# Optimization experiments

Measured on AMD Instinct MI355X. Metric: run time of the kernel, lower is better.

Reference implementation:

```python
import jax, jax.numpy as jnp
import numpy as np

VOCAB, EMB, HID = 10000, 512, 512
B, T = 32, 256


def _lstm_layer(x, W, U, b):
    # x: [B, T, D_in]; W: [D_in, 4H]; U: [H, 4H]; b: [4H]
    Bsz = x.shape[0]
    H = U.shape[0]
    xs = jnp.swapaxes(x, 0, 1)  # [T, B, D_in]

    def step(carry, xt):
        h, c = carry
        z = xt @ W + h @ U + b  # fused gate GEMM, [B, 4H]
        i, f, g, o = jnp.split(z, 4, axis=-1)
        i = jax.nn.sigmoid(i)
        f = jax.nn.sigmoid(f)
        g = jnp.tanh(g)
        o = jax.nn.sigmoid(o)
        c = f * c + i * g
        h = o * jnp.tanh(c)
        return (h, c), h

    init = (jnp.zeros((Bsz, H), x.dtype), jnp.zeros((Bsz, H), x.dtype))
    _, hs = jax.lax.scan(step, init, xs)  # hs: [T, B, H]
    return jnp.swapaxes(hs, 0, 1)  # [B, T, H]


def setup_inputs() -> dict:
    key = jax.random.key(0)
    ks = jax.random.split(key, 10)
    s = 1.0 / np.sqrt(HID)
    inp = {
        "tokens": jax.random.randint(ks[0], (B, T), 0, VOCAB, dtype=jnp.int32),
        "embedding": jax.random.normal(ks[1], (VOCAB, EMB), jnp.float32) * 0.02,
        "W0": jax.random.uniform(ks[2], (EMB, 4 * HID), jnp.float32, -s, s),
        "U0": jax.random.uniform(ks[3], (HID, 4 * HID), jnp.float32, -s, s),
        "b0": jnp.zeros((4 * HID,), jnp.float32),
        "W1": jax.random.uniform(ks[4], (HID, 4 * HID), jnp.float32, -s, s),
        "U1": jax.random.uniform(ks[5], (HID, 4 * HID), jnp.float32, -s, s),
        "b1": jnp.zeros((4 * HID,), jnp.float32),
        "W_out": jax.random.normal(ks[6], (HID, VOCAB), jnp.float32) * 0.02,
        "b_out": jnp.zeros((VOCAB,), jnp.float32),
    }
    return inp


def reference(tokens, embedding, W0, U0, b0, W1, U1, b1, W_out, b_out):
    x = embedding[tokens]            # [B, T, EMB]
    x = _lstm_layer(x, W0, U0, b0)   # [B, T, H]
    x = _lstm_layer(x, W1, U1, b1)   # [B, T, H]
    y = x.reshape(-1, HID) @ W_out + b_out  # [B*T, VOCAB]
    return y
```

## Files before the change

### kernel.cpp

```cpp
#include <hip/hip_runtime.h>
#include <math.h>

#define B_    32
#define T_    256
#define HID_  512
#define G4_   2048
#define VOC_  10000
#define NPAD_ 10112

typedef float f32x4 __attribute__((ext_vector_type(4)));
typedef short bf16x8 __attribute__((ext_vector_type(8)));
typedef unsigned short u16;
typedef u16 u16x8 __attribute__((ext_vector_type(8)));

#define AADD(p)  __hip_atomic_fetch_add((p), 1u, __ATOMIC_RELAXED, __HIP_MEMORY_SCOPE_AGENT)
#define ALOAD(p) __hip_atomic_load((p), __ATOMIC_RELAXED, __HIP_MEMORY_SCOPE_AGENT)

__device__ __forceinline__ void load4_coherent(const float* p0, const float* p1,
                                               const float* p2, const float* p3,
                                               f32x4& a, f32x4& b, f32x4& c, f32x4& d)
{
    asm volatile(
        "global_load_dwordx4 %0, %4, off sc0 sc1\n\t"
        "global_load_dwordx4 %1, %5, off sc0 sc1\n\t"
        "global_load_dwordx4 %2, %6, off sc0 sc1\n\t"
        "global_load_dwordx4 %3, %7, off sc0 sc1\n\t"
        "s_waitcnt vmcnt(0)"
        : "=&v"(a), "=&v"(b), "=&v"(c), "=&v"(d)
        : "v"(p0), "v"(p1), "v"(p2), "v"(p3)
        : "memory");
}
__device__ __forceinline__ void store_coherent(float* p, float x)
{
    asm volatile("global_store_dword %0, %1, off sc0 sc1" :: "v"(p), "v"(x) : "memory");
}

__device__ __forceinline__ float fsigm(float x)
{
    float e = exp2f(x * -1.4426950408889634f);
    return __builtin_amdgcn_rcpf(1.f + e);
}
__device__ __forceinline__ float ftanh(float x)
{
    float e = exp2f(x * 2.8853900817779268f);
    return 1.f - 2.f * __builtin_amdgcn_rcpf(e + 1.f);
}

__device__ __forceinline__ void bsplit(float x, u16& hi, u16& lo)
{
    union { float f; unsigned u; } a; a.f = x;
    unsigned r = a.u + 0x7FFFu + ((a.u >> 16) & 1u);
    hi = (u16)(r >> 16);
    union { unsigned u; float f; } hf; hf.u = ((unsigned)hi) << 16;
    union { float f; unsigned u; } b; b.f = x - hf.f;
    unsigned r2 = b.u + 0x7FFFu + ((b.u >> 16) & 1u);
    lo = (u16)(r2 >> 16);
}

__device__ __forceinline__ void wait_ge(unsigned* p, unsigned tgt)
{
    unsigned g = 0;
    while (ALOAD(p) < tgt) {
        __builtin_amdgcn_s_sleep(2);
        if (++g > 100000000u) break;
    }
}

__global__ __launch_bounds__(256)
void wsplit_k(const float* __restrict__ W, u16* __restrict__ Thi,
              u16* __restrict__ Tlo, int N)
{
    __shared__ float tile[64][68];
    const int tid = threadIdx.x;
    const int n0 = blockIdx.x * 64;
    const int k0 = blockIdx.y * 64;

    #pragma unroll
    for (int it = 0; it < 4; ++it) {
        int idx = it * 256 + tid;
        int kr = idx >> 4;
        int nc = (idx & 15) * 4;
        int n  = n0 + nc;
        float4 v = {0.f, 0.f, 0.f, 0.f};
        const float* wp = W + (size_t)(k0 + kr) * N + n;
        if (n + 3 < N) v = *(const float4*)wp;
        else {
            if (n + 0 < N) v.x = wp[0];
            if (n + 1 < N) v.y = wp[1];
            if (n + 2 < N) v.z = wp[2];
            if (n + 3 < N) v.w = wp[3];
        }
        tile[kr][nc + 0] = v.x; tile[kr][nc + 1] = v.y;
        tile[kr][nc + 2] = v.z; tile[kr][nc + 3] = v.w;
    }
    __syncthreads();

    #pragma unroll
    for (int it = 0; it < 2; ++it) {
        int idx = it * 256 + tid;
        int nr = idx >> 3;
        int kb = (idx & 7) * 8;
        u16x8 hv, lv;
        #pragma unroll
        for (int e = 0; e < 8; ++e) {
            u16 h, l;
            bsplit(tile[kb + e][nr], h, l);
            hv[e] = h; lv[e] = l;
        }
        size_t o = (size_t)(n0 + nr) * 512 + k0 + kb;
        *(u16x8*)(Thi + o) = hv;
        *(u16x8*)(Tlo + o) = lv;
    }
}

__global__ __launch_bounds__(256)
void gather_split_k(const int* __restrict__ tokens, const float* __restrict__ emb,
                    u16* __restrict__ Ahi, u16* __restrict__ Alo)
{
    const int r    = blockIdx.x * 4 + (threadIdx.x >> 6);
    const int lane = threadIdx.x & 63;
    const int tok  = tokens[(r & 31) * T_ + (r >> 5)];
    const float* src = emb + (size_t)tok * 512 + lane * 8;
    float4 v0 = *(const float4*)(src);
    float4 v1 = *(const float4*)(src + 4);
    const float vv[8] = {v0.x, v0.y, v0.z, v0.w, v1.x, v1.y, v1.z, v1.w};
    u16x8 hv, lv;
    #pragma unroll
    for (int e = 0; e < 8; ++e) { u16 h, l; bsplit(vv[e], h, l); hv[e] = h; lv[e] = l; }
    size_t o = (size_t)r * 512 + lane * 8;
    *(u16x8*)(Ahi + o) = hv;
    *(u16x8*)(Alo + o) = lv;
}

template<int MODE>
__global__ __launch_bounds__(256)
void gemm_bf16_k(const u16* __restrict__ Ahi, const u16* __restrict__ Alo,
                 const u16* __restrict__ Bhi, const u16* __restrict__ Blo,
                 const float* __restrict__ bias, float* __restrict__ C, int N)
{
    __shared__ u16 As[2][128 * 64];
    __shared__ u16 Bs[2][128 * 64];

    const int tid  = threadIdx.x;
    const int lane = tid & 63;
    const int wid  = tid >> 6;
    const int wm   = wid >> 1;
    const int wn   = wid & 1;
    const int m0   = blockIdx.y * 128;
    const int n0   = blockIdx.x * 128;

    f32x4 acc[4][4];
    #pragma unroll
    for (int i = 0; i < 4; ++i)
        #pragma unroll
        for (int j = 0; j < 4; ++j) acc[i][j] = (f32x4){0.f, 0.f, 0.f, 0.f};

    auto stage = [&](int s, int buf) {
        const int ksel = s >> 3;
        const int koff = (s & 7) * 64;
        const u16* Asrc = (ksel == 2) ? Alo : Ahi;
        const u16* Bsrc = (ksel == 1) ? Blo : Bhi;
        #pragma unroll
        for (int q = 0; q < 4; ++q) {
            const int u   = q * 256 + tid;
            const int row = u >> 3;
            const int kch = (u & 7) ^ (row & 7);
            const u16* ga = Asrc + (size_t)(m0 + row) * 512 + koff + kch * 8;
            const u16* gb = Bsrc + (size_t)(n0 + row) * 512 + koff + kch * 8;
            u16* la = &As[buf][(q * 256 + wid * 64) * 8];
            u16* lb = &Bs[buf][(q * 256 + wid * 64) * 8];
            __builtin_amdgcn_global_load_lds(
                (const __attribute__((address_space(1))) void*)ga,
                (__attribute__((address_space(3))) void*)la, 16, 0, 0);
            __builtin_amdgcn_global_load_lds(
                (const __attribute__((address_space(1))) void*)gb,
                (__attribute__((address_space(3))) void*)lb, 16, 0, 0);
        }
    };

    stage(0, 0);
    for (int s = 0; s < 24; ++s) {
        const int buf = s & 1;
        __syncthreads();
        if (s + 1 < 24) stage(s + 1, buf ^ 1);

        #pragma unroll
        for (int q = 0; q < 2; ++q) {
            bf16x8 af[4], bfr[4];
            #pragma unroll
            for (int mt = 0; mt < 4; ++mt) {
                const int r    = wm * 64 + mt * 16 + (lane & 15);
                const int slot = (q * 4 + (lane >> 4)) ^ (r & 7);
                af[mt] = *(const bf16x8*)&As[buf][r * 64 + slot * 8];
            }
            #pragma unroll
            for (int nt = 0; nt < 4; ++nt) {
                const int rn   = wn * 64 + nt * 16 + (lane & 15);
                const int slot = (q * 4 + (lane >> 4)) ^ (rn & 7);
                bfr[nt] = *(const bf16x8*)&Bs[buf][rn * 64 + slot * 8];
            }
            #pragma unroll
            for (int mt = 0; mt < 4; ++mt)
                #pragma unroll
                for (int nt = 0; nt < 4; ++nt)
                    acc[mt][nt] = __builtin_amdgcn_mfma_f32_16x16x32_bf16(
                        af[mt], bfr[nt], acc[mt][nt], 0, 0, 0);
        }
    }

    #pragma unroll
    for (int mt = 0; mt < 4; ++mt) {
        #pragma unroll
        for (int nt = 0; nt < 4; ++nt) {
            const int c = n0 + wn * 64 + nt * 16 + (lane & 15);
            #pragma unroll
            for (int j = 0; j < 4; ++j) {
                const int r = m0 + wm * 64 + mt * 16 + (lane >> 4) * 4 + j;
                float val = acc[mt][nt][j];
                if constexpr (MODE == 0) {
                    val += bias[c];
                    const int t = r >> 5, bgrp = (r >> 3) & 3, bb = r & 7;
                    const int g = c >> 9, jblk = (c & 511) >> 3, jjs = c & 7;
                    C[(((size_t)t * 4 + bgrp) * 64 + jblk) * 256 + bb * 32 + g * 8 + jjs] = val;
                } else {
                    if (c < VOC_) {
                        val += bias[c];
                        const size_t orow = (size_t)(r & 31) * T_ + (r >> 5);
                        C[orow * VOC_ + c] = val;
                    }
                }
            }
        }
    }
}

__global__ __launch_bounds__(256, 2)
void fused_rec_k(const float* __restrict__ G, const float* __restrict__ U0,
                 const float* __restrict__ W1, const float* __restrict__ U1,
                 const float* __restrict__ b1,
                 float* __restrict__ H0x,
                 u16* __restrict__ Ahi, u16* __restrict__ Alo,
                 float* __restrict__ h1buf,
                 unsigned* __restrict__ bar)
{
    __shared__ float lds[8 * 1152];

    const int tid  = threadIdx.x;
    const int role = blockIdx.x >> 8;
    const int blk  = blockIdx.x & 255;
    const int bg   = blk >> 6;
    const int cgr  = blk & 63;
    const int j0   = cgr * 8;
    const int b0   = bg * 8;

    const int jj  = tid >> 5;
    const int kc  = tid & 31;
    const int g_  = kc >> 3;
    const int bb_ = kc & 7;
    const int shard = cgr & 3;

    unsigned* shard0 = bar + (bg * 4 + shard) * 16;
    unsigned* root0  = bar + 256 + bg * 16;
    unsigned* shard1 = bar + 512 + (bg * 4 + shard) * 16;
    unsigned* root1  = bar + 768 + bg * 16;

    if (role == 0) {
        float u[4][16];
        #pragma unroll
        for (int g = 0; g < 4; ++g)
            #pragma unroll
            for (int kk = 0; kk < 16; ++kk)
                u[g][kk] = U0[(size_t)(kc * 16 + kk) * G4_ + (g << 9) + j0 + jj];

        const int gofs = bb_ * 32 + g_ * 8 + jj;
        float zpre = G[((size_t)bg * 64 + cgr) * 256 + gofs];
        float c_reg = 0.f;

        for (int t = 0; t < T_; ++t) {
            if (tid == 0 && t > 0) wait_ge(root0, 4u * (unsigned)t);
            __syncthreads();

            {
                const float* p[4]; float* dst[4];
                const float* hcur = H0x + (size_t)t * (B_ * HID_);
                #pragma unroll
                for (int q = 0; q < 4; ++q) {
                    int idx = q * 256 + tid;
                    int bL  = idx >> 7;
                    int k4  = idx & 127;
                    p[q]   = hcur + (b0 + bL) * HID_ + k4 * 4;
                    dst[q] = &lds[bL * 640 + (k4 >> 2) * 20 + (k4 & 3) * 4];
                }
                f32x4 v0, v1, v2, v3;
                load4_coherent(p[0], p[1], p[2], p[3], v0, v1, v2, v3);
                *(f32x4*)dst[0] = v0; *(f32x4*)dst[1] = v1;
                *(f32x4*)dst[2] = v2; *(f32x4*)dst[3] = v3;
            }
            __syncthreads();

            float zpre_next = 0.f;
            if (t + 1 < T_)
                zpre_next = G[((size_t)((t + 1) * 4 + bg) * 64 + cgr) * 256 + gofs];

            float v[32];
            #pragma unroll
            for (int s = 0; s < 32; ++s) v[s] = 0.f;
            #pragma unroll
            for (int bb = 0; bb < 8; ++bb) {
                const float* hp = &lds[bb * 640 + kc * 20];
                f32x4 h0v = *(const f32x4*)(hp + 0);
                f32x4 h1v = *(const f32x4*)(hp + 4);
                f32x4 h2v = *(const f32x4*)(hp + 8);
                f32x4 h3v = *(const f32x4*)(hp + 12);
                const float hh[16] = {h0v.x, h0v.y, h0v.z, h0v.w, h1v.x, h1v.y, h1v.z, h1v.w,
                                      h2v.x, h2v.y, h2v.z, h2v.w, h3v.x, h3v.y, h3v.z, h3v.w};
                #pragma unroll
                for (int g = 0; g < 4; ++g)
                    #pragma unroll
                    for (int kk = 0; kk < 16; ++kk)
                        v[g * 8 + bb] += u[g][kk] * hh[kk];
            }

            float a16[16];
            #pragma unroll
            for (int i = 0; i < 16; ++i) {
                float keep = (kc & 16) ? v[i + 16] : v[i];
                float give = (kc & 16) ? v[i]      : v[i + 16];
                a16[i] = keep + __shfl_xor(give, 16, 32);
            }
            float a8[8];
            #pragma unroll
            for (int i = 0; i < 8; ++i) {
                float keep = (kc & 8) ? a16[i + 8] : a16[i];
                float give = (kc & 8) ? a16[i]     : a16[i + 8];
                a8[i] = keep + __shfl_xor(give, 8, 32);
            }
            float a4[4];
            #pragma unroll
            for (int i = 0; i < 4; ++i) {
                float keep = (kc & 4) ? a8[i + 4] : a8[i];
                float give = (kc & 4) ? a8[i]     : a8[i + 4];
                a4[i] = keep + __shfl_xor(give, 4, 32);
            }
            float a2[2];
            #pragma unroll
            for (int i = 0; i < 2; ++i) {
                float keep = (kc & 2) ? a4[i + 2] : a4[i];
                float give = (kc & 2) ? a4[i]     : a4[i + 2];
                a2[i] = keep + __shfl_xor(give, 2, 32);
            }
            float keep1 = (kc & 1) ? a2[1] : a2[0];
            float give1 = (kc & 1) ? a2[0] : a2[1];
            float z = keep1 + __shfl_xor(give1, 1, 32) + zpre;
            zpre = zpre_next;

            float z8  = __shfl_xor(z, 8, 32);
            float z16 = __shfl_xor(z, 16, 32);
            float z24 = __shfl_xor(z, 24, 32);
            float i_ = fsigm(z);
            float f_ = fsigm(z8);
            float gg = ftanh(z16);
            float o_ = fsigm(z24);
            c_reg = f_ * c_reg + i_ * gg;
            float h_ = o_ * ftanh(c_reg);

            if (g_ == 0)
                store_coherent(&H0x[(size_t)(t + 1) * (B_ * HID_)
                                    + (b0 + bb_) * HID_ + j0 + jj], h_);

            __syncthreads();
            if (tid == 0) {
                unsigned old = AADD(shard0);
                if (old + 1u == 16u * (unsigned)(t + 1)) AADD(root0);
            }
        }
    } else {
        float u[4][32];
        #pragma unroll
        for (int g = 0; g < 4; ++g)
            #pragma unroll
            for (int kk = 0; kk < 32; ++kk) {
                const int K = kc * 32 + kk;
                u[g][kk] = (K < 512)
                    ? W1[(size_t)K * G4_ + (g << 9) + j0 + jj]
                    : U1[(size_t)(K - 512) * G4_ + (g << 9) + j0 + jj];
            }
        const float zb = b1[(g_ << 9) + j0 + jj];
        float c_reg = 0.f;

        for (int t = 0; t < T_; ++t) {
            if (tid == 0) {
                wait_ge(root0, 4u * (unsigned)(t + 1));
                if (t > 0) wait_ge(root1, 4u * (unsigned)t);
            }
            __syncthreads();

            {
                const float* xbase = H0x  + (size_t)(t + 1) * (B_ * HID_);
                const float* hbase = h1buf + (size_t)(t & 1) * (B_ * HID_);
                const float* p[8]; float* dst[8];
                const int k = tid * 4;
                #pragma unroll
                for (int q = 0; q < 8; ++q) {
                    p[q] = (k < 512) ? (xbase + (b0 + q) * HID_ + k)
                                     : (hbase + (b0 + q) * HID_ + (k - 512));
                    dst[q] = &lds[q * 1152 + (tid >> 3) * 36 + (tid & 7) * 4];
                }
                f32x4 v0, v1, v2, v3, v4, v5, v6, v7;
                load4_coherent(p[0], p[1], p[2], p[3], v0, v1, v2, v3);
                load4_coherent(p[4], p[5], p[6], p[7], v4, v5, v6, v7);
                *(f32x4*)dst[0] = v0; *(f32x4*)dst[1] = v1;
                *(f32x4*)dst[2] = v2; *(f32x4*)dst[3] = v3;
                *(f32x4*)dst[4] = v4; *(f32x4*)dst[5] = v5;
                *(f32x4*)dst[6] = v6; *(f32x4*)dst[7] = v7;
            }
            __syncthreads();

            float v[32];
            #pragma unroll
            for (int s = 0; s < 32; ++s) v[s] = 0.f;
            #pragma unroll
            for (int bb = 0; bb < 8; ++bb) {
                const float* hp = &lds[bb * 1152 + kc * 36];
                #pragma unroll
                for (int half = 0; half < 2; ++half) {
                    f32x4 h0v = *(const f32x4*)(hp + half * 16 + 0);
                    f32x4 h1v = *(const f32x4*)(hp + half * 16 + 4);
                    f32x4 h2v = *(const f32x4*)(hp + half * 16 + 8);
                    f32x4 h3v = *(const f32x4*)(hp + half * 16 + 12);
                    const float hh[16] = {h0v.x, h0v.y, h0v.z, h0v.w, h1v.x, h1v.y, h1v.z, h1v.w,
                                          h2v.x, h2v.y, h2v.z, h2v.w, h3v.x, h3v.y, h3v.z, h3v.w};
                    #pragma unroll
                    for (int g = 0; g < 4; ++g)
                        #pragma unroll
                        for (int kk = 0; kk < 16; ++kk)
                            v[g * 8 + bb] += u[g][half * 16 + kk] * hh[kk];
                }
            }

            float a16[16];
            #pragma unroll
            for (int i = 0; i < 16; ++i) {
                float keep = (kc & 16) ? v[i + 16] : v[i];
                float give = (kc & 16) ? v[i]      : v[i + 16];
                a16[i] = keep + __shfl_xor(give, 16, 32);
            }
            float a8[8];
            #pragma unroll
            for (int i = 0; i < 8; ++i) {
                float keep = (kc & 8) ? a16[i + 8] : a16[i];
                float give = (kc & 8) ? a16[i]     : a16[i + 8];
                a8[i] = keep + __shfl_xor(give, 8, 32);
            }
            float a4[4];
            #pragma unroll
            for (int i = 0; i < 4; ++i) {
                float keep = (kc & 4) ? a8[i + 4] : a8[i];
                float give = (kc & 4) ? a8[i]     : a8[i + 4];
                a4[i] = keep + __shfl_xor(give, 4, 32);
            }
            float a2[2];
            #pragma unroll
            for (int i = 0; i < 2; ++i) {
                float keep = (kc & 2) ? a4[i + 2] : a4[i];
                float give = (kc & 2) ? a4[i]     : a4[i + 2];
                a2[i] = keep + __shfl_xor(give, 2, 32);
            }
            float keep1 = (kc & 1) ? a2[1] : a2[0];
            float give1 = (kc & 1) ? a2[0] : a2[1];
            float z = keep1 + __shfl_xor(give1, 1, 32) + zb;

            float z8  = __shfl_xor(z, 8, 32);
            float z16 = __shfl_xor(z, 16, 32);
            float z24 = __shfl_xor(z, 24, 32);
            float i_ = fsigm(z);
            float f_ = fsigm(z8);
            float gg = ftanh(z16);
            float o_ = fsigm(z24);
            c_reg = f_ * c_reg + i_ * gg;
            float h_ = o_ * ftanh(c_reg);

            if (g_ == 0) {
                const int brow = b0 + bb_;
                store_coherent(&h1buf[(size_t)((t + 1) & 1) * (B_ * HID_)
                                      + brow * HID_ + j0 + jj], h_);
                u16 hi, lo; bsplit(h_, hi, lo);
                const size_t o = ((size_t)t * B_ + brow) * HID_ + j0 + jj;
                Ahi[o] = hi;
                Alo[o] = lo;
            }

            __syncthreads();
            if (tid == 0) {
                unsigned old = AADD(shard1);
                if (old + 1u == 16u * (unsigned)(t + 1)) AADD(root1);
            }
        }
    }
}

extern "C" void kernel_launch(void* const* d_in, const int* in_sizes, int n_in,
                              void* d_out, int out_size, void* d_ws, size_t ws_size,
                              hipStream_t stream)
{
    const int*   tokens = (const int*)  d_in[0];
    const float* emb    = (const float*)d_in[1];
    const float* W0     = (const float*)d_in[2];
    const float* U0     = (const float*)d_in[3];
    const float* b0     = (const float*)d_in[4];
    const float* W1     = (const float*)d_in[5];
    const float* U1     = (const float*)d_in[6];
    const float* b1     = (const float*)d_in[7];
    const float* Wout   = (const float*)d_in[8];
    const float* bout   = (const float*)d_in[9];
    float* out = (float*)d_out;

    float* G   = out;
    float* H0x = out + (size_t)8192 * 2048;

    u16* ws16 = (u16*)d_ws;
    size_t o = 0;
    u16* Ahi   = ws16 + o; o += (size_t)8192 * 512;
    u16* Alo   = ws16 + o; o += (size_t)8192 * 512;
    u16* W0Thi = ws16 + o; o += (size_t)G4_ * 512;
    u16* W0Tlo = ws16 + o; o += (size_t)G4_ * 512;
    u16* WoThi = ws16 + o; o += (size_t)NPAD_ * 512;
    u16* WoTlo = ws16 + o; o += (size_t)NPAD_ * 512;
    float*    h1buf = (float*)(ws16 + o);
    unsigned* bar   = (unsigned*)(h1buf + 2 * B_ * HID_);

    dim3 blk(256);

    wsplit_k<<<dim3(G4_ / 64, 8), blk, 0, stream>>>(W0, W0Thi, W0Tlo, G4_);
    wsplit_k<<<dim3(NPAD_ / 64, 8), blk, 0, stream>>>(Wout, WoThi, WoTlo, VOC_);
    gather_split_k<<<dim3(2048), blk, 0, stream>>>(tokens, emb, Ahi, Alo);

    gemm_bf16_k<0><<<dim3(G4_ / 128, 64), blk, 0, stream>>>(
        Ahi, Alo, W0Thi, W0Tlo, b0, G, G4_);

    hipMemsetAsync(H0x, 0, B_ * HID_ * sizeof(float), stream);
    hipMemsetAsync(h1buf, 0, B_ * HID_ * sizeof(float), stream);
    hipMemsetAsync(bar, 0, 1024 * sizeof(unsigned), stream);
    fused_rec_k<<<dim3(512), blk, 0, stream>>>(
        G, U0, W1, U1, b1, H0x, Ahi, Alo, h1buf, bar);

    gemm_bf16_k<1><<<dim3(NPAD_ / 128, 64), blk, 0, stream>>>(
        Ahi, Alo, WoThi, WoTlo, bout, out, NPAD_);
}
```

Before: 2.215 ms.

## Split layer-1 recurrence into separate input-projection and recurrent roles

The persistent recurrent kernel gains a third role. New blocks compute the layer-1 input projection x_t@W1+b1 into a G1 buffer, pipelined behind layer 0, so the layer-1 recurrent blocks only do h@U1 with half the K dimension. This shortens the critical path of the serial layer-1 recurrence. In exchange it launches 768 blocks at 3 per CU, which needs all of them co-resident for the spin barriers, and it adds extra global traffic and synchronization through G1.

```diff
diff --git a/kernel.cpp b/kernel.cpp
--- a/kernel.cpp
+++ b/kernel.cpp
@@ -7,6 +7,7 @@
 #define G4_   2048
 #define VOC_  10000
 #define NPAD_ 10112
+#define BH_   (B_ * HID_)
 
 typedef float f32x4 __attribute__((ext_vector_type(4)));
 typedef short bf16x8 __attribute__((ext_vector_type(8)));
@@ -29,6 +30,13 @@
         : "=&v"(a), "=&v"(b), "=&v"(c), "=&v"(d)
         : "v"(p0), "v"(p1), "v"(p2), "v"(p3)
         : "memory");
+}
+__device__ __forceinline__ float load_coherent_f32(const float* p)
+{
+    float v;
+    asm volatile("global_load_dword %0, %1, off sc0 sc1\n\ts_waitcnt vmcnt(0)"
+                 : "=v"(v) : "v"(p) : "memory");
+    return v;
 }
 __device__ __forceinline__ void store_coherent(float* p, float x)
 {
@@ -234,16 +242,17 @@
     }
 }
 
-__global__ __launch_bounds__(256, 2)
-void fused_rec_k(const float* __restrict__ G, const float* __restrict__ U0,
-                 const float* __restrict__ W1, const float* __restrict__ U1,
-                 const float* __restrict__ b1,
-                 float* __restrict__ H0x,
-                 u16* __restrict__ Ahi, u16* __restrict__ Alo,
-                 float* __restrict__ h1buf,
-                 unsigned* __restrict__ bar)
-{
-    __shared__ float lds[8 * 1152];
+__global__ __launch_bounds__(256, 3)
+void rec3_k(const float* __restrict__ G, const float* __restrict__ U0,
+            const float* __restrict__ W1, const float* __restrict__ U1,
+            const float* __restrict__ b1,
+            float* __restrict__ H0x,
+            float* __restrict__ G1,
+            u16* __restrict__ Ahi, u16* __restrict__ Alo,
+            float* __restrict__ h1buf,
+            unsigned* __restrict__ bar)
+{
+    __shared__ float lds[8 * 640];
 
     const int tid  = threadIdx.x;
     const int role = blockIdx.x >> 8;
@@ -257,102 +266,116 @@
     const int kc  = tid & 31;
     const int g_  = kc >> 3;
     const int bb_ = kc & 7;
-    const int shard = cgr & 3;
-
-    unsigned* shard0 = bar + (bg * 4 + shard) * 16;
-    unsigned* root0  = bar + 256 + bg * 16;
-    unsigned* shard1 = bar + 512 + (bg * 4 + shard) * 16;
-    unsigned* root1  = bar + 768 + bg * 16;
+    const int gofs = bb_ * 32 + g_ * 8 + jj;
+
+    unsigned* baseA = bar + (0 * 4 + bg) * 80;
+    unsigned* baseB = bar + (1 * 4 + bg) * 80;
+    unsigned* baseC = bar + (2 * 4 + bg) * 80;
+    unsigned* mybase  = (role == 0) ? baseA : (role == 1) ? baseB : baseC;
+    unsigned* myshard = mybase + (cgr & 3) * 16;
+    unsigned* myroot  = mybase + 64;
+    unsigned* rootA = baseA + 64;
+    unsigned* rootB = baseB + 64;
+    unsigned* rootC = baseC + 64;
+
+    const float* Usrc = (role == 0) ? U0 : (role == 1) ? W1 : U1;
+    float u[4][16];
+    #pragma unroll
+    for (int g = 0; g < 4; ++g)
+        #pragma unroll
+        for (int kk = 0; kk < 16; ++kk)
+            u[g][kk] = Usrc[(size_t)(kc * 16 + kk) * G4_ + (g << 9) + j0 + jj];
+
+    auto stage_tile = [&](const float* src) {
+        const float* p[4]; float* dst[4];
+        #pragma unroll
+        for (int q = 0; q < 4; ++q) {
+            int idx = q * 256 + tid;
+            int bL  = idx >> 7;
+            int k4  = idx & 127;
+            p[q]   = src + (b0 + bL) * HID_ + k4 * 4;
+            dst[q] = &lds[bL * 640 + (k4 >> 2) * 20 + (k4 & 3) * 4];
+        }
+        f32x4 v0, v1, v2, v3;
+        load4_coherent(p[0], p[1], p[2], p[3], v0, v1, v2, v3);
+        *(f32x4*)dst[0] = v0; *(f32x4*)dst[1] = v1;
+        *(f32x4*)dst[2] = v2; *(f32x4*)dst[3] = v3;
+    };
+
+    auto dot_reduce = [&]() -> float {
+        float v[32];
+        #pragma unroll
+        for (int s = 0; s < 32; ++s) v[s] = 0.f;
+        #pragma unroll
+        for (int bb = 0; bb < 8; ++bb) {
+            const float* hp = &lds[bb * 640 + kc * 20];
+            f32x4 h0v = *(const f32x4*)(hp + 0);
+            f32x4 h1v = *(const f32x4*)(hp + 4);
+            f32x4 h2v = *(const f32x4*)(hp + 8);
+            f32x4 h3v = *(const f32x4*)(hp + 12);
+            const float hh[16] = {h0v.x, h0v.y, h0v.z, h0v.w, h1v.x, h1v.y, h1v.z, h1v.w,
+                                  h2v.x, h2v.y, h2v.z, h2v.w, h3v.x, h3v.y, h3v.z, h3v.w};
+            #pragma unroll
+            for (int g = 0; g < 4; ++g)
+                #pragma unroll
+                for (int kk = 0; kk < 16; ++kk)
+                    v[g * 8 + bb] += u[g][kk] * hh[kk];
+        }
+        float a16[16];
+        #pragma unroll
+        for (int i = 0; i < 16; ++i) {
+            float keep = (kc & 16) ? v[i + 16] : v[i];
+            float give = (kc & 16) ? v[i]      : v[i + 16];
+            a16[i] = keep + __shfl_xor(give, 16, 32);
+        }
+        float a8[8];
+        #pragma unroll
+        for (int i = 0; i < 8; ++i) {
+            float keep = (kc & 8) ? a16[i + 8] : a16[i];
+            float give = (kc & 8) ? a16[i]     : a16[i + 8];
+            a8[i] = keep + __shfl_xor(give, 8, 32);
+        }
+        float a4[4];
+        #pragma unroll
+        for (int i = 0; i < 4; ++i) {
+            float keep = (kc & 4) ? a8[i + 4] : a8[i];
+            float give = (kc & 4) ? a8[i]     : a8[i + 4];
+            a4[i] = keep + __shfl_xor(give, 4, 32);
+        }
+        float a2[2];
+        #pragma unroll
+        for (int i = 0; i < 2; ++i) {
+            float keep = (kc & 2) ? a4[i + 2] : a4[i];
+            float give = (kc & 2) ? a4[i]     : a4[i + 2];
+            a2[i] = keep + __shfl_xor(give, 2, 32);
+        }
+        float keep1 = (kc & 1) ? a2[1] : a2[0];
+        float give1 = (kc & 1) ? a2[0] : a2[1];
+        return keep1 + __shfl_xor(give1, 1, 32);
+    };
+
+    auto arrive = [&](int t) {
+        if (tid == 0) {
+            unsigned old = AADD(myshard);
+            if (old + 1u == 16u * (unsigned)(t + 1)) AADD(myroot);
+        }
+    };
 
     if (role == 0) {
-        float u[4][16];
-        #pragma unroll
-        for (int g = 0; g < 4; ++g)
-            #pragma unroll
-            for (int kk = 0; kk < 16; ++kk)
-                u[g][kk] = U0[(size_t)(kc * 16 + kk) * G4_ + (g << 9) + j0 + jj];
-
-        const int gofs = bb_ * 32 + g_ * 8 + jj;
         float zpre = G[((size_t)bg * 64 + cgr) * 256 + gofs];
         float c_reg = 0.f;
-
         for (int t = 0; t < T_; ++t) {
-            if (tid == 0 && t > 0) wait_ge(root0, 4u * (unsigned)t);
-            __syncthreads();
-
-            {
-                const float* p[4]; float* dst[4];
-                const float* hcur = H0x + (size_t)t * (B_ * HID_);
-                #pragma unroll
-                for (int q = 0; q < 4; ++q) {
-                    int idx = q * 256 + tid;
-                    int bL  = idx >> 7;
-                    int k4  = idx & 127;
-                    p[q]   = hcur + (b0 + bL) * HID_ + k4 * 4;
-                    dst[q] = &lds[bL * 640 + (k4 >> 2) * 20 + (k4 & 3) * 4];
-                }
-                f32x4 v0, v1, v2, v3;
-                load4_coherent(p[0], p[1], p[2], p[3], v0, v1, v2, v3);
-                *(f32x4*)dst[0] = v0; *(f32x4*)dst[1] = v1;
-                *(f32x4*)dst[2] = v2; *(f32x4*)dst[3] = v3;
-            }
-            __syncthreads();
-
-            float zpre_next = 0.f;
+            if (tid == 0 && t > 0) wait_ge(rootA, 4u * (unsigned)t);
+            __syncthreads();
+            stage_tile(H0x + (size_t)t * BH_);
+            __syncthreads();
+
+            float zpn = 0.f;
             if (t + 1 < T_)
-                zpre_next = G[((size_t)((t + 1) * 4 + bg) * 64 + cgr) * 256 + gofs];
-
-            float v[32];
-            #pragma unroll
-            for (int s = 0; s < 32; ++s) v[s] = 0.f;
-            #pragma unroll
-            for (int bb = 0; bb < 8; ++bb) {
-                const float* hp = &lds[bb * 640 + kc * 20];
-                f32x4 h0v = *(const f32x4*)(hp + 0);
-                f32x4 h1v = *(const f32x4*)(hp + 4);
-                f32x4 h2v = *(const f32x4*)(hp + 8);
-                f32x4 h3v = *(const f32x4*)(hp + 12);
-                const float hh[16] = {h0v.x, h0v.y, h0v.z, h0v.w, h1v.x, h1v.y, h1v.z, h1v.w,
-                                      h2v.x, h2v.y, h2v.z, h2v.w, h3v.x, h3v.y, h3v.z, h3v.w};
-                #pragma unroll
-                for (int g = 0; g < 4; ++g)
-                    #pragma unroll
-                    for (int kk = 0; kk < 16; ++kk)
-                        v[g * 8 + bb] += u[g][kk] * hh[kk];
-            }
-
-            float a16[16];
-            #pragma unroll
-            for (int i = 0; i < 16; ++i) {
-                float keep = (kc & 16) ? v[i + 16] : v[i];
-                float give = (kc & 16) ? v[i]      : v[i + 16];
-                a16[i] = keep + __shfl_xor(give, 16, 32);
-            }
-            float a8[8];
-            #pragma unroll
-            for (int i = 0; i < 8; ++i) {
-                float keep = (kc & 8) ? a16[i + 8] : a16[i];
-                float give = (kc & 8) ? a16[i]     : a16[i + 8];
-                a8[i] = keep + __shfl_xor(give, 8, 32);
-            }
-            float a4[4];
-            #pragma unroll
-            for (int i = 0; i < 4; ++i) {
-                float keep = (kc & 4) ? a8[i + 4] : a8[i];
-                float give = (kc & 4) ? a8[i]     : a8[i + 4];
-                a4[i] = keep + __shfl_xor(give, 4, 32);
-            }
-            float a2[2];
-            #pragma unroll
-            for (int i = 0; i < 2; ++i) {
-                float keep = (kc & 2) ? a4[i + 2] : a4[i];
-                float give = (kc & 2) ? a4[i]     : a4[i + 2];
-                a2[i] = keep + __shfl_xor(give, 2, 32);
-            }
-            float keep1 = (kc & 1) ? a2[1] : a2[0];
-            float give1 = (kc & 1) ? a2[0] : a2[1];
-            float z = keep1 + __shfl_xor(give1, 1, 32) + zpre;
-            zpre = zpre_next;
+                zpn = G[(((size_t)(t + 1) * 4 + bg) * 64 + cgr) * 256 + gofs];
+
+            float z = dot_reduce() + zpre;
+            zpre = zpn;
 
             float z8  = __shfl_xor(z, 8, 32);
             float z16 = __shfl_xor(z, 16, 32);
@@ -365,110 +388,39 @@
             float h_ = o_ * ftanh(c_reg);
 
             if (g_ == 0)
-                store_coherent(&H0x[(size_t)(t + 1) * (B_ * HID_)
-                                    + (b0 + bb_) * HID_ + j0 + jj], h_);
-
-            __syncthreads();
-            if (tid == 0) {
-                unsigned old = AADD(shard0);
-                if (old + 1u == 16u * (unsigned)(t + 1)) AADD(root0);
-            }
+                store_coherent(&H0x[(size_t)(t + 1) * BH_ + (b0 + bb_) * HID_ + j0 + jj], h_);
+
+            __syncthreads();
+            arrive(t);
+        }
+    } else if (role == 1) {
+        const float zb = b1[(g_ << 9) + j0 + jj];
+        for (int t = 0; t < T_; ++t) {
+            if (tid == 0) wait_ge(rootA, 4u * (unsigned)(t + 1));
+            __syncthreads();
+            stage_tile(H0x + (size_t)(t + 1) * BH_);
+            __syncthreads();
+
+            float z = dot_reduce() + zb;
+            store_coherent(&G1[(((size_t)t * 4 + bg) * 64 + cgr) * 256 + gofs], z);
+
+            __syncthreads();
+            arrive(t);
         }
     } else {
-        float u[4][32];
-        #pragma unroll
-        for (int g = 0; g < 4; ++g)
-            #pragma unroll
-            for (int kk = 0; kk < 32; ++kk) {
-                const int K = kc * 32 + kk;
-                u[g][kk] = (K < 512)
-                    ? W1[(size_t)K * G4_ + (g << 9) + j0 + jj]
-                    : U1[(size_t)(K - 512) * G4_ + (g << 9) + j0 + jj];
-            }
-        const float zb = b1[(g_ << 9) + j0 + jj];
         float c_reg = 0.f;
-
         for (int t = 0; t < T_; ++t) {
             if (tid == 0) {
-                wait_ge(root0, 4u * (unsigned)(t + 1));
-                if (t > 0) wait_ge(root1, 4u * (unsigned)t);
+                wait_ge(rootB, 4u * (unsigned)(t + 1));
+                if (t > 0) wait_ge(rootC, 4u * (unsigned)t);
             }
             __syncthreads();
-
-            {
-                const float* xbase = H0x  + (size_t)(t + 1) * (B_ * HID_);
-                const float* hbase = h1buf + (size_t)(t & 1) * (B_ * HID_);
-                const float* p[8]; float* dst[8];
-                const int k = tid * 4;
-                #pragma unroll
-                for (int q = 0; q < 8; ++q) {
-                    p[q] = (k < 512) ? (xbase + (b0 + q) * HID_ + k)
-                                     : (hbase + (b0 + q) * HID_ + (k - 512));
-                    dst[q] = &lds[q * 1152 + (tid >> 3) * 36 + (tid & 7) * 4];
-                }
-                f32x4 v0, v1, v2, v3, v4, v5, v6, v7;
-                load4_coherent(p[0], p[1], p[2], p[3], v0, v1, v2, v3);
-                load4_coherent(p[4], p[5], p[6], p[7], v4, v5, v6, v7);
-                *(f32x4*)dst[0] = v0; *(f32x4*)dst[1] = v1;
-                *(f32x4*)dst[2] = v2; *(f32x4*)dst[3] = v3;
-                *(f32x4*)dst[4] = v4; *(f32x4*)dst[5] = v5;
-                *(f32x4*)dst[6] = v6; *(f32x4*)dst[7] = v7;
-            }
-            __syncthreads();
-
-            float v[32];
-            #pragma unroll
-            for (int s = 0; s < 32; ++s) v[s] = 0.f;
-            #pragma unroll
-            for (int bb = 0; bb < 8; ++bb) {
-                const float* hp = &lds[bb * 1152 + kc * 36];
-                #pragma unroll
-                for (int half = 0; half < 2; ++half) {
-                    f32x4 h0v = *(const f32x4*)(hp + half * 16 + 0);
-                    f32x4 h1v = *(const f32x4*)(hp + half * 16 + 4);
-                    f32x4 h2v = *(const f32x4*)(hp + half * 16 + 8);
-                    f32x4 h3v = *(const f32x4*)(hp + half * 16 + 12);
-                    const float hh[16] = {h0v.x, h0v.y, h0v.z, h0v.w, h1v.x, h1v.y, h1v.z, h1v.w,
-                                          h2v.x, h2v.y, h2v.z, h2v.w, h3v.x, h3v.y, h3v.z, h3v.w};
-                    #pragma unroll
-                    for (int g = 0; g < 4; ++g)
-                        #pragma unroll
-                        for (int kk = 0; kk < 16; ++kk)
-                            v[g * 8 + bb] += u[g][half * 16 + kk] * hh[kk];
-                }
-            }
-
-            float a16[16];
-            #pragma unroll
-            for (int i = 0; i < 16; ++i) {
-                float keep = (kc & 16) ? v[i + 16] : v[i];
-                float give = (kc & 16) ? v[i]      : v[i + 16];
-                a16[i] = keep + __shfl_xor(give, 16, 32);
-            }
-            float a8[8];
-            #pragma unroll
-            for (int i = 0; i < 8; ++i) {
-                float keep = (kc & 8) ? a16[i + 8] : a16[i];
-                float give = (kc & 8) ? a16[i]     : a16[i + 8];
-                a8[i] = keep + __shfl_xor(give, 8, 32);
-            }
-            float a4[4];
-            #pragma unroll
-            for (int i = 0; i < 4; ++i) {
-                float keep = (kc & 4) ? a8[i + 4] : a8[i];
-                float give = (kc & 4) ? a8[i]     : a8[i + 4];
-                a4[i] = keep + __shfl_xor(give, 4, 32);
-            }
-            float a2[2];
-            #pragma unroll
-            for (int i = 0; i < 2; ++i) {
-                float keep = (kc & 2) ? a4[i + 2] : a4[i];
-                float give = (kc & 2) ? a4[i]     : a4[i + 2];
-                a2[i] = keep + __shfl_xor(give, 2, 32);
-            }
-            float keep1 = (kc & 1) ? a2[1] : a2[0];
-            float give1 = (kc & 1) ? a2[0] : a2[1];
-            float z = keep1 + __shfl_xor(give1, 1, 32) + zb;
+            stage_tile(h1buf + (size_t)(t & 1) * BH_);
+            float g1v = load_coherent_f32(
+                G1 + (((size_t)t * 4 + bg) * 64 + cgr) * 256 + gofs);
+            __syncthreads();
+
+            float z = dot_reduce() + g1v;
 
             float z8  = __shfl_xor(z, 8, 32);
             float z16 = __shfl_xor(z, 16, 32);
@@ -482,8 +434,7 @@
 
             if (g_ == 0) {
                 const int brow = b0 + bb_;
-                store_coherent(&h1buf[(size_t)((t + 1) & 1) * (B_ * HID_)
-                                      + brow * HID_ + j0 + jj], h_);
+                store_coherent(&h1buf[(size_t)((t + 1) & 1) * BH_ + brow * HID_ + j0 + jj], h_);
                 u16 hi, lo; bsplit(h_, hi, lo);
                 const size_t o = ((size_t)t * B_ + brow) * HID_ + j0 + jj;
                 Ahi[o] = hi;
@@ -491,10 +442,7 @@
             }
 
             __syncthreads();
-            if (tid == 0) {
-                unsigned old = AADD(shard1);
-                if (old + 1u == 16u * (unsigned)(t + 1)) AADD(root1);
-            }
+            arrive(t);
         }
     }
 }
@@ -517,6 +465,7 @@
 
     float* G   = out;
     float* H0x = out + (size_t)8192 * 2048;
+    float* G1  = H0x + (size_t)(T_ + 1) * BH_;
 
     u16* ws16 = (u16*)d_ws;
     size_t o = 0;
@@ -527,7 +476,7 @@
     u16* WoThi = ws16 + o; o += (size_t)NPAD_ * 512;
     u16* WoTlo = ws16 + o; o += (size_t)NPAD_ * 512;
     float*    h1buf = (float*)(ws16 + o);
-    unsigned* bar   = (unsigned*)(h1buf + 2 * B_ * HID_);
+    unsigned* bar   = (unsigned*)(h1buf + 2 * BH_);
 
     dim3 blk(256);
 
@@ -538,11 +487,11 @@
     gemm_bf16_k<0><<<dim3(G4_ / 128, 64), blk, 0, stream>>>(
         Ahi, Alo, W0Thi, W0Tlo, b0, G, G4_);
 
-    hipMemsetAsync(H0x, 0, B_ * HID_ * sizeof(float), stream);
-    hipMemsetAsync(h1buf, 0, B_ * HID_ * sizeof(float), stream);
+    hipMemsetAsync(H0x, 0, BH_ * sizeof(float), stream);
+    hipMemsetAsync(h1buf, 0, BH_ * sizeof(float), stream);
     hipMemsetAsync(bar, 0, 1024 * sizeof(unsigned), stream);
-    fused_rec_k<<<dim3(512), blk, 0, stream>>>(
-        G, U0, W1, U1, b1, H0x, Ahi, Alo, h1buf, bar);
+    rec3_k<<<dim3(768), blk, 0, stream>>>(
+        G, U0, W1, U1, b1, H0x, G1, Ahi, Alo, h1buf, bar);
 
     gemm_bf16_k<1><<<dim3(NPAD_ / 128, 64), blk, 0, stream>>>(
         Ahi, Alo, WoThi, WoTlo, bout, out, NPAD_);
```

Result: slower. 3.583 ms (+61.8%).
